# Kernel optimization log

Measured on AMD Instinct MI355X. Metric: run time of the kernel, lower is better.

The kernel has to match this reference:

```python
import jax, jax.numpy as jnp
from jax import lax
import numpy as np

D_MODEL = 96; D_STATE = 16; SSM_RATIO = 2.0; D_CONV = 3; K = 4
D_INNER = int(SSM_RATIO * D_MODEL)      # 192
DT_RANK = -(-D_MODEL // 16)             # ceil(96/16) = 6
B_SZ = 4; H = 32; W = 32

# ---- zig-zag (snake) index helpers (static numpy) ----
def _snake_h(Hh, Ww):
    idx = np.tile(np.arange(Ww), (Hh, 1)); idx[1::2] = idx[1::2, ::-1]; return idx  # (H,W)

def _snake_v(Hh, Ww):
    idx = np.tile(np.arange(Hh)[:, None], (1, Ww)); idx[:, 1::2] = idx[::-1, 1::2]; return idx  # (H,W)

def _h_scan(x, d):
    Hh, Ww = x.shape[-2:]
    if d == 'left':
        x = jnp.flip(x, (-1, -2))
    return x[:, :, np.arange(Hh)[:, None], _snake_h(Hh, Ww)]

def _v_scan(x, d):
    Bb, Cc, Hh, Ww = x.shape
    if d == 'up':
        x = jnp.flip(x, (-1, -2))
    t = x[:, :, _snake_v(Hh, Ww), np.arange(Ww)[None, :]]  # gather along H per column
    return jnp.swapaxes(t, -1, -2).reshape(Bb, Cc, Hh, Ww)

def _h_merge(x, d):
    Hh, Ww = x.shape[-2:]
    t = x[:, :, np.arange(Hh)[:, None], _snake_h(Hh, Ww)]
    if d == 'left':
        t = jnp.flip(t, (-1, -2))
    return t

def _v_merge(x, d):
    Hh, Ww = x.shape[-2:]
    t2 = jnp.swapaxes(x, -1, -2)  # (B,C,W,H); requires H==W like the torch source
    t = t2[:, :, _snake_v(Hh, Ww), np.arange(Ww)[None, :]]
    if d == 'up':
        t = jnp.flip(t, (-1, -2))
    return t

def cross_scan(x):
    return jnp.stack([_v_scan(x, 'down'), _v_scan(x, 'up'), _h_scan(x, 'right'), _h_scan(x, 'left')], axis=1)

def cross_merge(ys):
    return (_v_merge(ys[:, 0], 'down') + _v_merge(ys[:, 1], 'up')
            + _h_merge(ys[:, 2], 'right') + _h_merge(ys[:, 3], 'left'))

def selective_scan(u, delta, A, Bs, Cs, Dp, delta_bias):
    # u,delta:(B,K,D,L)  A:(K,D,N)  Bs,Cs:(B,K,N,L)  Dp,delta_bias:(K,D)
    delta = jax.nn.softplus(delta + delta_bias[None, :, :, None])
    dA = jnp.exp(jnp.einsum('bkdl,kdn->lbkdn', delta, A))
    dBu = jnp.einsum('bkdl,bkdl,bknl->lbkdn', delta, u, Bs)
    Ct = jnp.moveaxis(Cs, -1, 0)  # (L,B,K,N)
    def step(h, inp):
        dA_t, dBu_t, c_t = inp
        h = dA_t * h + dBu_t
        return h, jnp.einsum('bkdn,bkn->bkd', h, c_t)
    h0 = jnp.zeros(dA.shape[1:], u.dtype)
    _, ys = lax.scan(step, h0, (dA, dBu, Ct))
    return jnp.moveaxis(ys, 0, -1) + Dp[None, :, :, None] * u  # (B,K,D,L)

def setup_inputs() -> dict:
    key = jax.random.key(0)
    ks = jax.random.split(key, 8)
    x = jax.random.normal(ks[0], (B_SZ, D_MODEL, H, W), jnp.float32)
    in_proj_w = jax.random.normal(ks[1], (2 * D_INNER, D_MODEL), jnp.float32) * (D_MODEL ** -0.5)
    conv_w = jax.random.normal(ks[2], (D_INNER, 1, D_CONV, D_CONV), jnp.float32) * 0.2  # depthwise
    conv_b = jnp.zeros((D_INNER,), jnp.float32)
    x_proj_w = jax.random.normal(ks[3], (K, DT_RANK + 2 * D_STATE, D_INNER), jnp.float32) * (D_INNER ** -0.5)
    s = DT_RANK ** -0.5
    dt_w = jax.random.uniform(ks[4], (K, D_INNER, DT_RANK), jnp.float32, -s, s)
    dt = jax.random.uniform(ks[5], (K, D_INNER), jnp.float32, 0.001, 0.1)
    dt_b = jnp.log(jnp.expm1(dt))  # inverse softplus, as in dt_init
    A_logs = jnp.tile(jnp.log(jnp.arange(1, D_STATE + 1, dtype=jnp.float32)), (K * D_INNER, 1))
    Ds = jnp.ones((K * D_INNER,), jnp.float32)
    gn_gamma = jnp.ones((D_INNER,), jnp.float32)
    gn_beta = jnp.zeros((D_INNER,), jnp.float32)
    out_proj_w = jax.random.normal(ks[6], (D_MODEL, D_INNER), jnp.float32) * (D_INNER ** -0.5)
    return {'x': x, 'in_proj_w': in_proj_w, 'conv_w': conv_w, 'conv_b': conv_b,
            'x_proj_w': x_proj_w, 'dt_w': dt_w, 'dt_b': dt_b, 'A_logs': A_logs, 'Ds': Ds,
            'gn_gamma': gn_gamma, 'gn_beta': gn_beta, 'out_proj_w': out_proj_w}

def reference(x, in_proj_w, conv_w, conv_b, x_proj_w, dt_w, dt_b, A_logs, Ds, gn_gamma, gn_beta, out_proj_w):
    Bb, _, Hh, Ww = x.shape; L = Hh * Ww
    xz = jnp.einsum('bchw,oc->bohw', x, in_proj_w)          # in_proj (1x1 conv, no bias)
    xx, z = jnp.split(xz, 2, axis=1)
    z = jax.nn.silu(z)
    xx = lax.conv_general_dilated(xx, conv_w, (1, 1), 'SAME', feature_group_count=D_INNER,
                                  dimension_numbers=('NCHW', 'OIHW', 'NCHW')) + conv_b[None, :, None, None]
    xx = jax.nn.silu(xx)
    xs = cross_scan(xx).reshape(Bb, K, D_INNER, L)          # 4-direction zig-zag scan
    x_dbl = jnp.einsum('bkdl,kcd->bkcl', xs, x_proj_w)
    dts = jnp.einsum('bkrl,kdr->bkdl', x_dbl[:, :, :DT_RANK], dt_w)
    Bs = x_dbl[:, :, DT_RANK:DT_RANK + D_STATE]
    Cs = x_dbl[:, :, DT_RANK + D_STATE:]
    A = -jnp.exp(A_logs).reshape(K, D_INNER, D_STATE)
    y = selective_scan(xs, dts, A, Bs, Cs, Ds.reshape(K, D_INNER), dt_b)
    y = cross_merge(y.reshape(Bb, K, D_INNER, Hh, Ww))       # (B,D,H,W)
    # out_norm: GroupNorm(1, d_inner) == layernorm over (C,H,W) per sample
    mu = jnp.mean(y, axis=(1, 2, 3), keepdims=True)
    var = jnp.var(y, axis=(1, 2, 3), keepdims=True)
    y = (y - mu) * lax.rsqrt(var + 1e-6)
    y = y * gn_gamma[None, :, None, None] + gn_beta[None, :, None, None]
    y = y * z
    return jnp.einsum('bchw,oc->bohw', y, out_proj_w)
```

## Files before the change

### kernel.cpp

```cpp
#include <hip/hip_runtime.h>
#include <math.h>

#define Bsz 4
#define DM 96
#define DI 192
#define NS 16
#define RK 6
#define KK 4
#define HH 32
#define WW 32
#define LL 1024
#define NC 32
#define CS 32

__device__ __forceinline__ float silu_f(float x) { return x / (1.f + __expf(-x)); }

__device__ __forceinline__ int hw_of_l(int k, int l) {
    int a = l >> 5, r = l & 31;
    int m = (a & 1) ? 31 - r : r;
    int h, w;
    if (k < 2) { w = a; h = m; }
    else       { h = a; w = m; }
    if (k & 1) { h = 31 - h; w = 31 - w; }
    return h * 32 + w;
}

__global__ void in_proj_k(const float* __restrict__ x, const float* __restrict__ w,
                          float* __restrict__ xx, float* __restrict__ zs,
                          float* __restrict__ stats) {
    int bi = blockIdx.x;
    int t = threadIdx.x;
    if (bi == 0 && t < 2 * Bsz) stats[t] = 0.f;
    int lb = bi & 3;
    int og = (bi >> 2) % 48;
    int b = bi / 192;
    int l = lb * 256 + t;
    const float* xb = x + (size_t)b * DM * LL + l;
    float acc[8];
#pragma unroll
    for (int g = 0; g < 8; g++) acc[g] = 0.f;
    for (int c = 0; c < DM; c++) {
        float xv = xb[(size_t)c * LL];
#pragma unroll
        for (int g = 0; g < 8; g++)
            acc[g] = fmaf(xv, w[(size_t)(og * 8 + g) * DM + c], acc[g]);
    }
#pragma unroll
    for (int g = 0; g < 8; g++) {
        int o = og * 8 + g;
        if (o < DI) xx[((size_t)b * DI + o) * LL + l] = acc[g];
        else        zs[((size_t)b * DI + (o - DI)) * LL + l] = silu_f(acc[g]);
    }
}

__global__ void convT_k(const float* __restrict__ xx, const float* __restrict__ cw,
                        const float* __restrict__ cb, float* __restrict__ xxT) {
    __shared__ float tile[32][65];
    int bi = blockIdx.x;
    int h0 = bi % 32;
    int dt = (bi / 32) % 3;
    int b = bi / 96;
    int d0 = dt * 64;
    int t = threadIdx.x;
    int wi = t & 31, dg = t >> 5;

#pragma unroll
    for (int pass = 0; pass < 8; pass++) {
        int di = pass * 8 + dg;
        int d = d0 + di;
        const float* xp = xx + ((size_t)b * DI + d) * LL;
        const float* wp = cw + d * 9;
        float acc = cb[d];
#pragma unroll
        for (int kh = 0; kh < 3; kh++) {
            int hh = h0 + kh - 1;
            if (hh < 0 || hh >= HH) continue;
#pragma unroll
            for (int kw = 0; kw < 3; kw++) {
                int ww2 = wi + kw - 1;
                if (ww2 < 0 || ww2 >= WW) continue;
                acc = fmaf(xp[hh * WW + ww2], wp[kh * 3 + kw], acc);
            }
        }
        tile[wi][di] = silu_f(acc);
    }
    __syncthreads();

    int di = t & 63, w4 = t >> 6;
#pragma unroll
    for (int rep = 0; rep < 8; rep++) {
        int w2 = rep * 4 + w4;
        xxT[((size_t)b * LL + h0 * 32 + w2) * DI + d0 + di] = tile[w2][di];
    }
}

__global__ void __launch_bounds__(512)
xdbl_k(const float* __restrict__ xxT, const float* __restrict__ xpw,
       float* __restrict__ xdbl) {
    __shared__ float tile[64 * 193];
    int blk = blockIdx.x;
    int bk = blk >> 4, lt = blk & 15;
    int k = bk & 3, b = bk >> 2;
    int t = threadIdx.x;

    const float* xb = xxT + (size_t)b * LL * DI;
#pragma unroll
    for (int i = 0; i < 6; i++) {
        int j4 = t + i * 512;
        int lr = j4 / 48;
        int d4 = j4 % 48;
        int hw = hw_of_l(k, lt * 64 + lr);
        float4 v = ((const float4*)(xb + (size_t)hw * DI))[d4];
        float* dst = &tile[lr * 193 + d4 * 4];
        dst[0] = v.x; dst[1] = v.y; dst[2] = v.z; dst[3] = v.w;
    }
    __syncthreads();

    int ll = t & 63;
    int cg = t >> 6;
    int c0 = cg * 5;
    int wlim = (c0 + 5 <= 38) ? 5 : (38 - c0);
    const float* wk = xpw + (size_t)k * 38 * DI;

    float acc[5];
#pragma unroll
    for (int j = 0; j < 5; j++) acc[j] = 0.f;
    const float* xrow = &tile[ll * 193];
#pragma unroll 4
    for (int d = 0; d < DI; d++) {
        float xv = xrow[d];
#pragma unroll
        for (int j = 0; j < 5; j++) {
            int cc = c0 + j; cc = (cc > 37) ? 37 : cc;
            acc[j] = fmaf(xv, wk[(size_t)cc * DI + d], acc[j]);
        }
    }
    float* orow = xdbl + ((size_t)bk * LL + lt * 64 + ll) * 38;
#pragma unroll
    for (int j = 0; j < 5; j++)
        if (j < wlim) orow[c0 + j] = acc[j];
}

__global__ void scan_p1(const float* __restrict__ xxT, const float* __restrict__ xdbl,
                        const float* __restrict__ dtw_g, const float* __restrict__ dtb_g,
                        const float* __restrict__ Alog,
                        float* __restrict__ Pst, float* __restrict__ Hloc) {
    int blk = blockIdx.x;
    int bk = blk / NC, c = blk % NC;
    int k = bk & 3, b = bk >> 2;
    int d = threadIdx.x;
    int kd = k * DI + d;

    float A[NS];
#pragma unroll
    for (int n = 0; n < NS; n++) A[n] = -__expf(Alog[(size_t)kd * NS + n]);
    float dtw[RK];
#pragma unroll
    for (int r = 0; r < RK; r++) dtw[r] = dtw_g[(size_t)kd * RK + r];
    float dtb = dtb_g[kd];

    float h[NS], P[NS];
#pragma unroll
    for (int n = 0; n < NS; n++) { h[n] = 0.f; P[n] = 1.f; }

    const float* xdbase = xdbl + ((size_t)bk * LL + c * CS) * 38;
    const float* xb = xxT + (size_t)b * LL * DI;

    for (int s = 0; s < CS; s++) {
        const float* xd = xdbase + s * 38;
        int hw = hw_of_l(k, c * CS + s);
        float u = xb[(size_t)hw * DI + d];
        float dt = dtb;
#pragma unroll
        for (int r = 0; r < RK; r++) dt = fmaf(xd[r], dtw[r], dt);
        dt = (dt > 20.f) ? dt : __logf(1.f + __expf(dt));
        float du = dt * u;
#pragma unroll
        for (int n = 0; n < NS; n++) {
            float a = __expf(dt * A[n]);
            h[n] = fmaf(a, h[n], du * xd[6 + n]);
            P[n] *= a;
        }
    }
    size_t base = ((size_t)blk * DI + d) * NS;
#pragma unroll
    for (int n = 0; n < NS; n++) { Pst[base + n] = P[n]; Hloc[base + n] = h[n]; }
}

__global__ void scan_mid(const float* __restrict__ Pst, float* __restrict__ Hloc) {
    int gid = blockIdx.x * 256 + threadIdx.x;
    int bk = gid / 1536;
    int j = gid % 1536;
    const float2* Pp = (const float2*)(Pst + (size_t)bk * NC * (DI * NS)) + j;
    float2* Hp = (float2*)(Hloc + (size_t)bk * NC * (DI * NS)) + j;
    const int S = (DI * NS) / 2;

    float2 h = make_float2(0.f, 0.f);
    float2 P[4], L[4];
#pragma unroll
    for (int q = 0; q < 4; q++) { P[q] = Pp[(size_t)q * S]; L[q] = Hp[(size_t)q * S]; }
    for (int c = 0; c < NC; c += 4) {
        float2 Pn[4], Ln[4];
        if (c + 4 < NC) {
#pragma unroll
            for (int q = 0; q < 4; q++) {
                Pn[q] = Pp[(size_t)(c + 4 + q) * S];
                Ln[q] = Hp[(size_t)(c + 4 + q) * S];
            }
        }
#pragma unroll
        for (int q = 0; q < 4; q++) {
            Hp[(size_t)(c + q) * S] = h;
            h.x = fmaf(P[q].x, h.x, L[q].x);
            h.y = fmaf(P[q].y, h.y, L[q].y);
        }
#pragma unroll
        for (int q = 0; q < 4; q++) { P[q] = Pn[q]; L[q] = Ln[q]; }
    }
}

__global__ void scan_p3(const float* __restrict__ xxT, const float* __restrict__ xdbl,
                        const float* __restrict__ dtw_g, const float* __restrict__ dtb_g,
                        const float* __restrict__ Alog, const float* __restrict__ Ds,
                        const float* __restrict__ Hin, float* __restrict__ ysm) {
    int blk = blockIdx.x;
    int bk = blk / NC, c = blk % NC;
    int k = bk & 3, b = bk >> 2;
    int d = threadIdx.x;
    int kd = k * DI + d;

    float A[NS];
#pragma unroll
    for (int n = 0; n < NS; n++) A[n] = -__expf(Alog[(size_t)kd * NS + n]);
    float dtw[RK];
#pragma unroll
    for (int r = 0; r < RK; r++) dtw[r] = dtw_g[(size_t)kd * RK + r];
    float dtb = dtb_g[kd];
    float Dp = Ds[kd];

    float h[NS];
    size_t hbase = ((size_t)blk * DI + d) * NS;
#pragma unroll
    for (int n = 0; n < NS; n++) h[n] = Hin[hbase + n];

    const float* xdbase = xdbl + ((size_t)bk * LL + c * CS) * 38;
    const float* xb = xxT + (size_t)b * LL * DI;
    float* yk = ysm + (size_t)bk * LL * DI;

    for (int s = 0; s < CS; s++) {
        const float* xd = xdbase + s * 38;
        int hw = hw_of_l(k, c * CS + s);
        float u = xb[(size_t)hw * DI + d];
        float dt = dtb;
#pragma unroll
        for (int r = 0; r < RK; r++) dt = fmaf(xd[r], dtw[r], dt);
        dt = (dt > 20.f) ? dt : __logf(1.f + __expf(dt));
        float du = dt * u;
        float y = 0.f;
#pragma unroll
        for (int n = 0; n < NS; n++) {
            float a = __expf(dt * A[n]);
            h[n] = fmaf(a, h[n], du * xd[6 + n]);
            y = fmaf(h[n], xd[22 + n], y);
        }
        yk[(size_t)hw * DI + d] = fmaf(Dp, u, y);
    }
}

#define MT 16
__global__ void merge_k(const float* __restrict__ ysm, float* __restrict__ ym,
                        float* __restrict__ stats) {
    __shared__ float tile[MT][DI + 1];
    __shared__ float sh1[3], sh2[3];
    int b = blockIdx.y;
    int hw0 = blockIdx.x * MT;
    int d = threadIdx.x;
    const float* yb = ysm + (size_t)b * KK * LL * DI;

    float s1 = 0.f, s2 = 0.f;
#pragma unroll
    for (int hwi = 0; hwi < MT; hwi++) {
        int hw = hw0 + hwi;
        float v = yb[((size_t)0 * LL + hw) * DI + d]
                + yb[((size_t)1 * LL + hw) * DI + d]
                + yb[((size_t)2 * LL + hw) * DI + d]
                + yb[((size_t)3 * LL + hw) * DI + d];
        tile[hwi][d] = v;
        s1 += v; s2 = fmaf(v, v, s2);
    }
#pragma unroll
    for (int off = 32; off > 0; off >>= 1) {
        s1 += __shfl_down(s1, off);
        s2 += __shfl_down(s2, off);
    }
    int lane = threadIdx.x & 63, wid = threadIdx.x >> 6;
    if (lane == 0) { sh1[wid] = s1; sh2[wid] = s2; }
    __syncthreads();
    if (threadIdx.x == 0) {
        atomicAdd(&stats[b * 2],     sh1[0] + sh1[1] + sh1[2]);
        atomicAdd(&stats[b * 2 + 1], sh2[0] + sh2[1] + sh2[2]);
    }
#pragma unroll
    for (int rep = 0; rep < MT; rep++) {
        int j = rep * DI + threadIdx.x;
        int d2 = j >> 4;
        int hwi = j & (MT - 1);
        ym[((size_t)b * DI + d2) * LL + hw0 + hwi] = tile[hwi][d2];
    }
}

__global__ void yz_k(const float* __restrict__ ym, const float* __restrict__ zs,
                     const float* __restrict__ g, const float* __restrict__ be,
                     const float* __restrict__ stats, float* __restrict__ yz) {
    int idx = blockIdx.x * 256 + threadIdx.x;
    int c = (idx >> 10) % DI;
    int b = idx / (LL * DI);
    const float Ninv = 1.f / (float)(DI * LL);
    float mu = stats[b * 2] * Ninv;
    float var = stats[b * 2 + 1] * Ninv - mu * mu;
    float rstd = rsqrtf(var + 1e-6f);
    float v = (ym[idx] - mu) * rstd * g[c] + be[c];
    yz[idx] = v * zs[idx];
}

__global__ void out_k(const float* __restrict__ yz, const float* __restrict__ wo,
                      float* __restrict__ out) {
    int bi = blockIdx.x;
    int t = threadIdx.x;
    int lb = bi & 3;
    int og = (bi >> 2) % 24;
    int b = bi / 96;
    int l = lb * 256 + t;
    const float* yb = yz + (size_t)b * DI * LL + l;
    float acc[4];
#pragma unroll
    for (int g = 0; g < 4; g++) acc[g] = 0.f;
    for (int c = 0; c < DI; c++) {
        float yv = yb[(size_t)c * LL];
#pragma unroll
        for (int g = 0; g < 4; g++)
            acc[g] = fmaf(yv, wo[(size_t)(og * 4 + g) * DI + c], acc[g]);
    }
#pragma unroll
    for (int g = 0; g < 4; g++)
        out[((size_t)b * DM + og * 4 + g) * LL + l] = acc[g];
}

extern "C" void kernel_launch(void* const* d_in, const int* in_sizes, int n_in,
                              void* d_out, int out_size, void* d_ws, size_t ws_size,
                              hipStream_t stream) {
    const float* x    = (const float*)d_in[0];
    const float* ipw  = (const float*)d_in[1];
    const float* cw   = (const float*)d_in[2];
    const float* cb   = (const float*)d_in[3];
    const float* xpw  = (const float*)d_in[4];
    const float* dtw  = (const float*)d_in[5];
    const float* dtb  = (const float*)d_in[6];
    const float* Alog = (const float*)d_in[7];
    const float* Ds   = (const float*)d_in[8];
    const float* gng  = (const float*)d_in[9];
    const float* gnb  = (const float*)d_in[10];
    const float* opw  = (const float*)d_in[11];
    float* out = (float*)d_out;

    float* ws = (float*)d_ws;
    const size_t o_xx   = 0;
    const size_t o_zs   = o_xx   + (size_t)Bsz * DI * LL;
    const size_t o_xxT  = o_zs   + (size_t)Bsz * DI * LL;
    const size_t o_xdbl = o_xxT  + (size_t)Bsz * LL * DI;
    const size_t o_P    = o_xdbl + (size_t)Bsz * KK * LL * 38;
    const size_t o_H    = o_P    + (size_t)Bsz * KK * NC * DI * NS;
    const size_t o_ysm  = o_H    + (size_t)Bsz * KK * NC * DI * NS;
    const size_t o_st   = o_ysm  + (size_t)Bsz * KK * LL * DI;

    float* xx    = ws + o_xx;
    float* zs    = ws + o_zs;
    float* xxT   = ws + o_xxT;
    float* xdbl  = ws + o_xdbl;
    float* Pst   = ws + o_P;
    float* Hst   = ws + o_H;
    float* ysm   = ws + o_ysm;
    float* stats = ws + o_st;
    float* ym = xx;
    float* yz = Pst;

    hipLaunchKernelGGL(in_proj_k, dim3(768), dim3(256), 0, stream, x, ipw, xx, zs, stats);
    hipLaunchKernelGGL(convT_k, dim3(384), dim3(256), 0, stream, xx, cw, cb, xxT);
    hipLaunchKernelGGL(xdbl_k, dim3(256), dim3(512), 0, stream, xxT, xpw, xdbl);
    hipLaunchKernelGGL(scan_p1, dim3(Bsz * KK * NC), dim3(192), 0, stream,
                       xxT, xdbl, dtw, dtb, Alog, Pst, Hst);
    hipLaunchKernelGGL(scan_mid, dim3(96), dim3(256), 0, stream, Pst, Hst);
    hipLaunchKernelGGL(scan_p3, dim3(Bsz * KK * NC), dim3(192), 0, stream,
                       xxT, xdbl, dtw, dtb, Alog, Ds, Hst, ysm);
    hipLaunchKernelGGL(merge_k, dim3(LL / MT, Bsz), dim3(192), 0, stream, ysm, ym, stats);
    hipLaunchKernelGGL(yz_k, dim3(3072), dim3(256), 0, stream, ym, zs, gng, gnb, stats, yz);
    hipLaunchKernelGGL(out_k, dim3(384), dim3(256), 0, stream, yz, opw, out);
}
```

Baseline: 211.8 us.

## Fuse chunked scan phases into one cooperative kernel and fold norm into out-proj

New measurement: 449.5 us. 2.12x slower.

```diff
diff --git a/kernel.cpp b/kernel.cpp
--- a/kernel.cpp
+++ b/kernel.cpp
@@ -1,5 +1,8 @@
 #include <hip/hip_runtime.h>
+#include <hip/hip_cooperative_groups.h>
 #include <math.h>
+
+namespace cg = cooperative_groups;
 
 #define Bsz 4
 #define DM 96
@@ -141,14 +144,37 @@
         if (j < wlim) orow[c0 + j] = acc[j];
 }
 
-__global__ void scan_p1(const float* __restrict__ xxT, const float* __restrict__ xdbl,
-                        const float* __restrict__ dtw_g, const float* __restrict__ dtb_g,
-                        const float* __restrict__ Alog,
-                        float* __restrict__ Pst, float* __restrict__ Hloc) {
+__global__ void __launch_bounds__(192)
+megascan_k(const float* __restrict__ xxT, const float* __restrict__ xdbl,
+           const float* __restrict__ dtw_g, const float* __restrict__ dtb_g,
+           const float* __restrict__ Alog, const float* __restrict__ Ds,
+           float* __restrict__ Pst, float* __restrict__ Hst,
+           float* __restrict__ ysm) {
+    cg::grid_group grid = cg::this_grid();
+    __shared__ float u_tile[CS * 193];
+    __shared__ float xd_tile[CS * 38];
+    __shared__ float dt_tile[CS * 192];
+
     int blk = blockIdx.x;
-    int bk = blk / NC, c = blk % NC;
+    int bk = blk >> 5, c = blk & 31;
     int k = bk & 3, b = bk >> 2;
-    int d = threadIdx.x;
+    int t = threadIdx.x;
+
+    const float* xb = xxT + (size_t)b * LL * DI;
+#pragma unroll
+    for (int i = 0; i < 8; i++) {
+        int j4 = t + i * 192;
+        int s = j4 / 48, d4 = j4 % 48;
+        int hw = hw_of_l(k, c * CS + s);
+        float4 v = ((const float4*)(xb + (size_t)hw * DI))[d4];
+        float* dst = &u_tile[s * 193 + d4 * 4];
+        dst[0] = v.x; dst[1] = v.y; dst[2] = v.z; dst[3] = v.w;
+    }
+    const float* xdsrc = xdbl + ((size_t)bk * LL + c * CS) * 38;
+    for (int i = t; i < CS * 38; i += 192) xd_tile[i] = xdsrc[i];
+    __syncthreads();
+
+    int d = t;
     int kd = k * DI + d;
 
     float A[NS];
@@ -158,23 +184,20 @@
 #pragma unroll
     for (int r = 0; r < RK; r++) dtw[r] = dtw_g[(size_t)kd * RK + r];
     float dtb = dtb_g[kd];
+    float Dp = Ds[kd];
 
     float h[NS], P[NS];
 #pragma unroll
     for (int n = 0; n < NS; n++) { h[n] = 0.f; P[n] = 1.f; }
 
-    const float* xdbase = xdbl + ((size_t)bk * LL + c * CS) * 38;
-    const float* xb = xxT + (size_t)b * LL * DI;
-
     for (int s = 0; s < CS; s++) {
-        const float* xd = xdbase + s * 38;
-        int hw = hw_of_l(k, c * CS + s);
-        float u = xb[(size_t)hw * DI + d];
+        const float* xd = &xd_tile[s * 38];
         float dt = dtb;
 #pragma unroll
         for (int r = 0; r < RK; r++) dt = fmaf(xd[r], dtw[r], dt);
         dt = (dt > 20.f) ? dt : __logf(1.f + __expf(dt));
-        float du = dt * u;
+        dt_tile[s * 192 + d] = dt;
+        float du = dt * u_tile[s * 193 + d];
 #pragma unroll
         for (int n = 0; n < NS; n++) {
             float a = __expf(dt * A[n]);
@@ -184,77 +207,53 @@
     }
     size_t base = ((size_t)blk * DI + d) * NS;
 #pragma unroll
-    for (int n = 0; n < NS; n++) { Pst[base + n] = P[n]; Hloc[base + n] = h[n]; }
-}
-
-__global__ void scan_mid(const float* __restrict__ Pst, float* __restrict__ Hloc) {
-    int gid = blockIdx.x * 256 + threadIdx.x;
-    int bk = gid / 1536;
-    int j = gid % 1536;
-    const float2* Pp = (const float2*)(Pst + (size_t)bk * NC * (DI * NS)) + j;
-    float2* Hp = (float2*)(Hloc + (size_t)bk * NC * (DI * NS)) + j;
-    const int S = (DI * NS) / 2;
-
-    float2 h = make_float2(0.f, 0.f);
-    float2 P[4], L[4];
-#pragma unroll
-    for (int q = 0; q < 4; q++) { P[q] = Pp[(size_t)q * S]; L[q] = Hp[(size_t)q * S]; }
-    for (int c = 0; c < NC; c += 4) {
-        float2 Pn[4], Ln[4];
-        if (c + 4 < NC) {
+    for (int n = 0; n < NS; n++) { Pst[base + n] = P[n]; Hst[base + n] = h[n]; }
+
+    __threadfence();
+    grid.sync();
+
+    int gid = blk * 192 + t;
+    if (gid < Bsz * KK * 1536) {
+        int mbk = gid / 1536;
+        int j = gid % 1536;
+        const float2* Pp = (const float2*)(Pst + (size_t)mbk * NC * (DI * NS)) + j;
+        float2* Hp = (float2*)(Hst + (size_t)mbk * NC * (DI * NS)) + j;
+        const int S = (DI * NS) / 2;
+
+        float2 hh = make_float2(0.f, 0.f);
+        float2 Pr[4], Lr[4];
+#pragma unroll
+        for (int q = 0; q < 4; q++) { Pr[q] = Pp[(size_t)q * S]; Lr[q] = Hp[(size_t)q * S]; }
+        for (int cc = 0; cc < NC; cc += 4) {
+            float2 Pn[4], Ln[4];
+            if (cc + 4 < NC) {
+#pragma unroll
+                for (int q = 0; q < 4; q++) {
+                    Pn[q] = Pp[(size_t)(cc + 4 + q) * S];
+                    Ln[q] = Hp[(size_t)(cc + 4 + q) * S];
+                }
+            }
 #pragma unroll
             for (int q = 0; q < 4; q++) {
-                Pn[q] = Pp[(size_t)(c + 4 + q) * S];
-                Ln[q] = Hp[(size_t)(c + 4 + q) * S];
+                Hp[(size_t)(cc + q) * S] = hh;
+                hh.x = fmaf(Pr[q].x, hh.x, Lr[q].x);
+                hh.y = fmaf(Pr[q].y, hh.y, Lr[q].y);
             }
-        }
-#pragma unroll
-        for (int q = 0; q < 4; q++) {
-            Hp[(size_t)(c + q) * S] = h;
-            h.x = fmaf(P[q].x, h.x, L[q].x);
-            h.y = fmaf(P[q].y, h.y, L[q].y);
-        }
-#pragma unroll
-        for (int q = 0; q < 4; q++) { P[q] = Pn[q]; L[q] = Ln[q]; }
-    }
-}
-
-__global__ void scan_p3(const float* __restrict__ xxT, const float* __restrict__ xdbl,
-                        const float* __restrict__ dtw_g, const float* __restrict__ dtb_g,
-                        const float* __restrict__ Alog, const float* __restrict__ Ds,
-                        const float* __restrict__ Hin, float* __restrict__ ysm) {
-    int blk = blockIdx.x;
-    int bk = blk / NC, c = blk % NC;
-    int k = bk & 3, b = bk >> 2;
-    int d = threadIdx.x;
-    int kd = k * DI + d;
-
-    float A[NS];
-#pragma unroll
-    for (int n = 0; n < NS; n++) A[n] = -__expf(Alog[(size_t)kd * NS + n]);
-    float dtw[RK];
-#pragma unroll
-    for (int r = 0; r < RK; r++) dtw[r] = dtw_g[(size_t)kd * RK + r];
-    float dtb = dtb_g[kd];
-    float Dp = Ds[kd];
-
-    float h[NS];
-    size_t hbase = ((size_t)blk * DI + d) * NS;
-#pragma unroll
-    for (int n = 0; n < NS; n++) h[n] = Hin[hbase + n];
-
-    const float* xdbase = xdbl + ((size_t)bk * LL + c * CS) * 38;
-    const float* xb = xxT + (size_t)b * LL * DI;
+#pragma unroll
+            for (int q = 0; q < 4; q++) { Pr[q] = Pn[q]; Lr[q] = Ln[q]; }
+        }
+    }
+    __threadfence();
+    grid.sync();
+
+#pragma unroll
+    for (int n = 0; n < NS; n++) h[n] = Hst[base + n];
     float* yk = ysm + (size_t)bk * LL * DI;
 
     for (int s = 0; s < CS; s++) {
-        const float* xd = xdbase + s * 38;
-        int hw = hw_of_l(k, c * CS + s);
-        float u = xb[(size_t)hw * DI + d];
-        float dt = dtb;
-#pragma unroll
-        for (int r = 0; r < RK; r++) dt = fmaf(xd[r], dtw[r], dt);
-        dt = (dt > 20.f) ? dt : __logf(1.f + __expf(dt));
+        const float* xd = &xd_tile[s * 38];
+        float dt = dt_tile[s * 192 + d];
+        float u = u_tile[s * 193 + d];
         float du = dt * u;
         float y = 0.f;
 #pragma unroll
@@ -263,6 +262,7 @@
             h[n] = fmaf(a, h[n], du * xd[6 + n]);
             y = fmaf(h[n], xd[22 + n], y);
         }
+        int hw = hw_of_l(k, c * CS + s);
         yk[(size_t)hw * DI + d] = fmaf(Dp, u, y);
     }
 }
@@ -309,41 +309,37 @@
     }
 }
 
-__global__ void yz_k(const float* __restrict__ ym, const float* __restrict__ zs,
-                     const float* __restrict__ g, const float* __restrict__ be,
-                     const float* __restrict__ stats, float* __restrict__ yz) {
-    int idx = blockIdx.x * 256 + threadIdx.x;
-    int c = (idx >> 10) % DI;
-    int b = idx / (LL * DI);
+__global__ void outz_k(const float* __restrict__ ym, const float* __restrict__ zs,
+                       const float* __restrict__ g, const float* __restrict__ be,
+                       const float* __restrict__ stats, const float* __restrict__ wo,
+                       float* __restrict__ out) {
+    int bi = blockIdx.x;
+    int t = threadIdx.x;
+    int lb = bi & 3;
+    int og = (bi >> 2) % 24;
+    int b = bi / 96;
+    int l = lb * 256 + t;
+
     const float Ninv = 1.f / (float)(DI * LL);
     float mu = stats[b * 2] * Ninv;
     float var = stats[b * 2 + 1] * Ninv - mu * mu;
     float rstd = rsqrtf(var + 1e-6f);
-    float v = (ym[idx] - mu) * rstd * g[c] + be[c];
-    yz[idx] = v * zs[idx];
-}
-
-__global__ void out_k(const float* __restrict__ yz, const float* __restrict__ wo,
-                      float* __restrict__ out) {
-    int bi = blockIdx.x;
-    int t = threadIdx.x;
-    int lb = bi & 3;
-    int og = (bi >> 2) % 24;
-    int b = bi / 96;
-    int l = lb * 256 + t;
-    const float* yb = yz + (size_t)b * DI * LL + l;
+
+    const float* yb = ym + (size_t)b * DI * LL + l;
+    const float* zb = zs + (size_t)b * DI * LL + l;
     float acc[4];
 #pragma unroll
-    for (int g = 0; g < 4; g++) acc[g] = 0.f;
+    for (int gg = 0; gg < 4; gg++) acc[gg] = 0.f;
     for (int c = 0; c < DI; c++) {
-        float yv = yb[(size_t)c * LL];
-#pragma unroll
-        for (int g = 0; g < 4; g++)
-            acc[g] = fmaf(yv, wo[(size_t)(og * 4 + g) * DI + c], acc[g]);
-    }
-#pragma unroll
-    for (int g = 0; g < 4; g++)
-        out[((size_t)b * DM + og * 4 + g) * LL + l] = acc[g];
+        float v = (yb[(size_t)c * LL] - mu) * rstd * g[c] + be[c];
+        float yv = v * zb[(size_t)c * LL];
+#pragma unroll
+        for (int gg = 0; gg < 4; gg++)
+            acc[gg] = fmaf(yv, wo[(size_t)(og * 4 + gg) * DI + c], acc[gg]);
+    }
+#pragma unroll
+    for (int gg = 0; gg < 4; gg++)
+        out[((size_t)b * DM + og * 4 + gg) * LL + l] = acc[gg];
 }
 
 extern "C" void kernel_launch(void* const* d_in, const int* in_sizes, int n_in,
@@ -382,17 +378,16 @@
     float* ysm   = ws + o_ysm;
     float* stats = ws + o_st;
     float* ym = xx;
-    float* yz = Pst;
 
     hipLaunchKernelGGL(in_proj_k, dim3(768), dim3(256), 0, stream, x, ipw, xx, zs, stats);
     hipLaunchKernelGGL(convT_k, dim3(384), dim3(256), 0, stream, xx, cw, cb, xxT);
     hipLaunchKernelGGL(xdbl_k, dim3(256), dim3(512), 0, stream, xxT, xpw, xdbl);
-    hipLaunchKernelGGL(scan_p1, dim3(Bsz * KK * NC), dim3(192), 0, stream,
-                       xxT, xdbl, dtw, dtb, Alog, Pst, Hst);
-    hipLaunchKernelGGL(scan_mid, dim3(96), dim3(256), 0, stream, Pst, Hst);
-    hipLaunchKernelGGL(scan_p3, dim3(Bsz * KK * NC), dim3(192), 0, stream,
-                       xxT, xdbl, dtw, dtb, Alog, Ds, Hst, ysm);
+
+    void* ka[] = {(void*)&xxT, (void*)&xdbl, (void*)&dtw, (void*)&dtb,
+                  (void*)&Alog, (void*)&Ds, (void*)&Pst, (void*)&Hst, (void*)&ysm};
+    hipLaunchCooperativeKernel((const void*)megascan_k, dim3(Bsz * KK * NC), dim3(192),
+                               ka, 0, stream);
+
     hipLaunchKernelGGL(merge_k, dim3(LL / MT, Bsz), dim3(192), 0, stream, ysm, ym, stats);
-    hipLaunchKernelGGL(yz_k, dim3(3072), dim3(256), 0, stream, ym, zs, gng, gnb, stats, yz);
-    hipLaunchKernelGGL(out_k, dim3(384), dim3(256), 0, stream, yz, opw, out);
-}
+    hipLaunchKernelGGL(outz_k, dim3(384), dim3(256), 0, stream, ym, zs, gng, gnb, stats, opw, out);
+}
```

## Fold chunk-carry scan into scan pass and fuse groupnorm-gate into out projection

Applied to the files above, without the earlier changes.

After: 232.9 us. 1.1x slower.

```diff
diff --git a/kernel.cpp b/kernel.cpp
--- a/kernel.cpp
+++ b/kernel.cpp
@@ -182,47 +182,18 @@
             P[n] *= a;
         }
     }
-    size_t base = ((size_t)blk * DI + d) * NS;
-#pragma unroll
-    for (int n = 0; n < NS; n++) { Pst[base + n] = P[n]; Hloc[base + n] = h[n]; }
-}
-
-__global__ void scan_mid(const float* __restrict__ Pst, float* __restrict__ Hloc) {
-    int gid = blockIdx.x * 256 + threadIdx.x;
-    int bk = gid / 1536;
-    int j = gid % 1536;
-    const float2* Pp = (const float2*)(Pst + (size_t)bk * NC * (DI * NS)) + j;
-    float2* Hp = (float2*)(Hloc + (size_t)bk * NC * (DI * NS)) + j;
-    const int S = (DI * NS) / 2;
-
-    float2 h = make_float2(0.f, 0.f);
-    float2 P[4], L[4];
-#pragma unroll
-    for (int q = 0; q < 4; q++) { P[q] = Pp[(size_t)q * S]; L[q] = Hp[(size_t)q * S]; }
-    for (int c = 0; c < NC; c += 4) {
-        float2 Pn[4], Ln[4];
-        if (c + 4 < NC) {
-#pragma unroll
-            for (int q = 0; q < 4; q++) {
-                Pn[q] = Pp[(size_t)(c + 4 + q) * S];
-                Ln[q] = Hp[(size_t)(c + 4 + q) * S];
-            }
-        }
-#pragma unroll
-        for (int q = 0; q < 4; q++) {
-            Hp[(size_t)(c + q) * S] = h;
-            h.x = fmaf(P[q].x, h.x, L[q].x);
-            h.y = fmaf(P[q].y, h.y, L[q].y);
-        }
-#pragma unroll
-        for (int q = 0; q < 4; q++) { P[q] = Pn[q]; L[q] = Ln[q]; }
-    }
-}
-
-__global__ void scan_p3(const float* __restrict__ xxT, const float* __restrict__ xdbl,
-                        const float* __restrict__ dtw_g, const float* __restrict__ dtb_g,
-                        const float* __restrict__ Alog, const float* __restrict__ Ds,
-                        const float* __restrict__ Hin, float* __restrict__ ysm) {
+    if (c < NC - 1) {
+        size_t base = ((size_t)blk * DI + d) * NS;
+#pragma unroll
+        for (int n = 0; n < NS; n++) { Pst[base + n] = P[n]; Hloc[base + n] = h[n]; }
+    }
+}
+
+__global__ void scan_p23(const float* __restrict__ xxT, const float* __restrict__ xdbl,
+                         const float* __restrict__ dtw_g, const float* __restrict__ dtb_g,
+                         const float* __restrict__ Alog, const float* __restrict__ Ds,
+                         const float* __restrict__ Pst, const float* __restrict__ Hloc,
+                         float* __restrict__ ysm) {
     int blk = blockIdx.x;
     int bk = blk / NC, c = blk % NC;
     int k = bk & 3, b = bk >> 2;
@@ -239,9 +210,17 @@
     float Dp = Ds[kd];
 
     float h[NS];
-    size_t hbase = ((size_t)blk * DI + d) * NS;
-#pragma unroll
-    for (int n = 0; n < NS; n++) h[n] = Hin[hbase + n];
+#pragma unroll
+    for (int n = 0; n < NS; n++) h[n] = 0.f;
+    for (int cc = 0; cc < c; cc++) {
+        size_t a = (((size_t)bk * NC + cc) * DI + d) * NS;
+#pragma unroll
+        for (int n = 0; n < NS; n++) {
+            float p  = Pst[a + n];
+            float hl = Hloc[a + n];
+            h[n] = fmaf(p, h[n], hl);
+        }
+    }
 
     const float* xdbase = xdbl + ((size_t)bk * LL + c * CS) * 38;
     const float* xb = xxT + (size_t)b * LL * DI;
@@ -309,41 +288,37 @@
     }
 }
 
-__global__ void yz_k(const float* __restrict__ ym, const float* __restrict__ zs,
-                     const float* __restrict__ g, const float* __restrict__ be,
-                     const float* __restrict__ stats, float* __restrict__ yz) {
-    int idx = blockIdx.x * 256 + threadIdx.x;
-    int c = (idx >> 10) % DI;
-    int b = idx / (LL * DI);
-    const float Ninv = 1.f / (float)(DI * LL);
-    float mu = stats[b * 2] * Ninv;
-    float var = stats[b * 2 + 1] * Ninv - mu * mu;
-    float rstd = rsqrtf(var + 1e-6f);
-    float v = (ym[idx] - mu) * rstd * g[c] + be[c];
-    yz[idx] = v * zs[idx];
-}
-
-__global__ void out_k(const float* __restrict__ yz, const float* __restrict__ wo,
-                      float* __restrict__ out) {
+__global__ void outz_k(const float* __restrict__ ym, const float* __restrict__ zs,
+                       const float* __restrict__ g, const float* __restrict__ be,
+                       const float* __restrict__ stats, const float* __restrict__ wo,
+                       float* __restrict__ out) {
     int bi = blockIdx.x;
     int t = threadIdx.x;
     int lb = bi & 3;
     int og = (bi >> 2) % 24;
     int b = bi / 96;
     int l = lb * 256 + t;
-    const float* yb = yz + (size_t)b * DI * LL + l;
+
+    const float Ninv = 1.f / (float)(DI * LL);
+    float mu = stats[b * 2] * Ninv;
+    float var = stats[b * 2 + 1] * Ninv - mu * mu;
+    float rstd = rsqrtf(var + 1e-6f);
+
+    const float* yb = ym + (size_t)b * DI * LL + l;
+    const float* zb = zs + (size_t)b * DI * LL + l;
     float acc[4];
 #pragma unroll
-    for (int g = 0; g < 4; g++) acc[g] = 0.f;
+    for (int gg = 0; gg < 4; gg++) acc[gg] = 0.f;
     for (int c = 0; c < DI; c++) {
-        float yv = yb[(size_t)c * LL];
-#pragma unroll
-        for (int g = 0; g < 4; g++)
-            acc[g] = fmaf(yv, wo[(size_t)(og * 4 + g) * DI + c], acc[g]);
-    }
-#pragma unroll
-    for (int g = 0; g < 4; g++)
-        out[((size_t)b * DM + og * 4 + g) * LL + l] = acc[g];
+        float v = (yb[(size_t)c * LL] - mu) * rstd * g[c] + be[c];
+        float yv = v * zb[(size_t)c * LL];
+#pragma unroll
+        for (int gg = 0; gg < 4; gg++)
+            acc[gg] = fmaf(yv, wo[(size_t)(og * 4 + gg) * DI + c], acc[gg]);
+    }
+#pragma unroll
+    for (int gg = 0; gg < 4; gg++)
+        out[((size_t)b * DM + og * 4 + gg) * LL + l] = acc[gg];
 }
 
 extern "C" void kernel_launch(void* const* d_in, const int* in_sizes, int n_in,
@@ -382,17 +357,14 @@
     float* ysm   = ws + o_ysm;
     float* stats = ws + o_st;
     float* ym = xx;
-    float* yz = Pst;
 
     hipLaunchKernelGGL(in_proj_k, dim3(768), dim3(256), 0, stream, x, ipw, xx, zs, stats);
     hipLaunchKernelGGL(convT_k, dim3(384), dim3(256), 0, stream, xx, cw, cb, xxT);
     hipLaunchKernelGGL(xdbl_k, dim3(256), dim3(512), 0, stream, xxT, xpw, xdbl);
     hipLaunchKernelGGL(scan_p1, dim3(Bsz * KK * NC), dim3(192), 0, stream,
                        xxT, xdbl, dtw, dtb, Alog, Pst, Hst);
-    hipLaunchKernelGGL(scan_mid, dim3(96), dim3(256), 0, stream, Pst, Hst);
-    hipLaunchKernelGGL(scan_p3, dim3(Bsz * KK * NC), dim3(192), 0, stream,
-                       xxT, xdbl, dtw, dtb, Alog, Ds, Hst, ysm);
+    hipLaunchKernelGGL(scan_p23, dim3(Bsz * KK * NC), dim3(192), 0, stream,
+                       xxT, xdbl, dtw, dtb, Alog, Ds, Pst, Hst, ysm);
     hipLaunchKernelGGL(merge_k, dim3(LL / MT, Bsz), dim3(192), 0, stream, ysm, ym, stats);
-    hipLaunchKernelGGL(yz_k, dim3(3072), dim3(256), 0, stream, ym, zs, gng, gnb, stats, yz);
-    hipLaunchKernelGGL(out_k, dim3(384), dim3(256), 0, stream, yz, opw, out);
-}
+    hipLaunchKernelGGL(outz_k, dim3(384), dim3(256), 0, stream, ym, zs, gng, gnb, stats, opw, out);
+}
```
